# Kernel optimization log

Hardware: AMD Instinct MI355X
Metric: run time of the kernel (lower is better)

The kernel has to match this reference:

```python
import jax, jax.numpy as jnp
import numpy as np

H = 1024        # hidden_size
NH = 16         # num_heads
HD = H // NH    # head_dim
DFF = 4 * H
SCALE = HD ** -0.5
EPS = 1e-5


def _ln(x, g, b):
    m = jnp.mean(x, axis=-1, keepdims=True)
    v = jnp.var(x, axis=-1, keepdims=True)
    return (x - m) * jax.lax.rsqrt(v + EPS) * g + b


def _heads(t, B):
    # [B, S, H] -> [B, NH, S, HD]
    return t.reshape(B, -1, NH, HD).transpose(0, 2, 1, 3)


def _merge(t, B):
    # [B, NH, S, HD] -> [B, S, H]
    return t.transpose(0, 2, 1, 3).reshape(B, -1, H)


def _attn(q, k, v):
    s = jnp.einsum('bhqd,bhkd->bhqk', q, k) * SCALE
    p = jax.nn.softmax(s, axis=-1)
    p = jnp.nan_to_num(p, nan=0.0)
    return jnp.einsum('bhqk,bhkd->bhqd', p, v)


def setup_inputs() -> dict:
    key = jax.random.key(0)
    ks = jax.random.split(key, 16)
    std = (2.0 / (5 * H)) ** 0.5
    B, S, SI = 2, 2048, 256
    d = {
        'x': jax.random.normal(ks[0], (B, S, H), jnp.float32),
        'image_features': jax.random.normal(ks[1], (B, SI, H), jnp.float32),
    }
    names = ['sq', 'sk', 'sv', 'so', 'cq', 'ck', 'cv', 'co']
    for i, n in enumerate(names):
        d['W_' + n] = std * jax.random.normal(ks[2 + i], (H, H), jnp.float32)
        d['b_' + n] = jnp.zeros((H,), jnp.float32)
    d['W_ff1'] = std * jax.random.normal(ks[10], (H, DFF), jnp.float32)
    d['b_ff1'] = jnp.zeros((DFF,), jnp.float32)
    d['W_ff2'] = std * jax.random.normal(ks[11], (DFF, H), jnp.float32)
    d['b_ff2'] = jnp.zeros((H,), jnp.float32)
    for n in ['ln1', 'ln2', 'ln3']:
        d['g_' + n] = jnp.ones((H,), jnp.float32)
        d['b_' + n] = jnp.zeros((H,), jnp.float32)
    return d


def reference(x, image_features,
              W_sq, b_sq, W_sk, b_sk, W_sv, b_sv, W_so, b_so,
              W_cq, b_cq, W_ck, b_ck, W_cv, b_cv, W_co, b_co,
              W_ff1, b_ff1, W_ff2, b_ff2,
              g_ln1, b_ln1, g_ln2, b_ln2, g_ln3, b_ln3):
    B = x.shape[0]
    x = x * 0.1
    img = image_features * 0.1

    # --- self attention (pre-norm) ---
    nx = _ln(x, g_ln1, b_ln1)
    q = _heads(nx @ W_sq + b_sq, B)
    k = _heads(nx @ W_sk + b_sk, B)
    v = _heads(nx @ W_sv + b_sv, B)
    so = _merge(_attn(q, k, v), B) @ W_so + b_so
    x = x + so

    # --- cross attention (pre-norm) ---
    nx = _ln(x, g_ln2, b_ln2)
    q = _heads(nx @ W_cq + b_cq, B)
    k = _heads(img @ W_ck + b_ck, B)
    v = _heads(img @ W_cv + b_cv, B)
    co = _merge(_attn(q, k, v), B) @ W_co + b_co
    x = x + co

    # --- feed forward (pre-norm) ---
    nx = _ln(x, g_ln3, b_ln3)
    ff = jax.nn.gelu(nx @ W_ff1 + b_ff1, approximate=False) @ W_ff2 + b_ff2
    x = x + ff
    return x * 10.0
```

## Files before the change

### kernel.cpp

```cpp
#include <hip/hip_runtime.h>
#include <hip/hip_bf16.h>

typedef __bf16 bf16;
typedef __bf16 bf16x4 __attribute__((ext_vector_type(4)));
typedef __bf16 bf16x8 __attribute__((ext_vector_type(8)));
typedef float  f32x4  __attribute__((ext_vector_type(4)));
typedef float  f32x16 __attribute__((ext_vector_type(16)));
typedef int    int4v  __attribute__((ext_vector_type(4)));

#define H_DIM 1024
#define NHEAD 16
#define HD    64
#define QSCL 0.18033688011112042f

__device__ __forceinline__ void gload_lds16(const bf16* g, bf16* l) {
    __builtin_amdgcn_global_load_lds((const __attribute__((address_space(1))) void*)g,
                                     (__attribute__((address_space(3))) void*)l, 16, 0, 0);
}

__device__ __forceinline__ unsigned cvtpk_bf16(float lo, float hi) {
    unsigned r;
    asm volatile("v_cvt_pk_bf16_f32 %0, %1, %2" : "=v"(r) : "v"(lo), "v"(hi));
    return r;
}

__device__ __forceinline__ void wconv_body(const float* __restrict__ W,
                                           bf16* __restrict__ Wt, int K, int N,
                                           int bx, int by, int t) {
    __shared__ float tile[64][65];
    const int n0 = bx * 64, k0 = by * 64;
#pragma unroll
    for (int p = 0; p < 4; ++p) {
        int lin = p * 1024 + t * 4;
        int r = lin >> 6, c = lin & 63;
        f32x4 v = *(const f32x4*)(W + (size_t)(k0 + r) * N + n0 + c);
        tile[r][c]     = v[0];
        tile[r][c + 1] = v[1];
        tile[r][c + 2] = v[2];
        tile[r][c + 3] = v[3];
    }
    __syncthreads();
#pragma unroll
    for (int p = 0; p < 4; ++p) {
        int lin = p * 1024 + t * 4;
        int rn = lin >> 6, ck = lin & 63;
        bf16x4 o;
#pragma unroll
        for (int j = 0; j < 4; ++j) o[j] = (bf16)tile[ck + j][rn];
        *(bf16x4*)(Wt + (size_t)(n0 + rn) * K + k0 + ck) = o;
    }
}

__global__ __launch_bounds__(256) void wconv_kernel(const float* __restrict__ W,
                                                    bf16* __restrict__ Wt,
                                                    int K, int N) {
    wconv_body(W, Wt, K, N, blockIdx.x, blockIdx.y, threadIdx.x);
}

struct WPtrs { const float* w[8]; bf16* o[8]; };
__global__ __launch_bounds__(256) void wconv8_kernel(WPtrs p) {
    const int m = blockIdx.z;
    wconv_body(p.w[m], p.o[m], 1024, 1024, blockIdx.x, blockIdx.y, threadIdx.x);
}

__global__ __launch_bounds__(256) void ln_kernel(const float* __restrict__ in, float inScale,
                                                 const float* __restrict__ g,
                                                 const float* __restrict__ b,
                                                 bf16* __restrict__ out) {
    const int row = blockIdx.x, t = threadIdx.x;
    const float* p = in + (size_t)row * H_DIM;
    f32x4 v = *(const f32x4*)(p + t * 4);
    v *= inScale;
    float s1 = v[0] + v[1] + v[2] + v[3];
    float s2 = v[0] * v[0] + v[1] * v[1] + v[2] * v[2] + v[3] * v[3];
#pragma unroll
    for (int m = 1; m < 64; m <<= 1) {
        s1 += __shfl_xor(s1, m);
        s2 += __shfl_xor(s2, m);
    }
    __shared__ float red[8];
    const int wave = t >> 6;
    if ((t & 63) == 0) { red[wave * 2] = s1; red[wave * 2 + 1] = s2; }
    __syncthreads();
    s1 = red[0] + red[2] + red[4] + red[6];
    s2 = red[1] + red[3] + red[5] + red[7];
    float mean = s1 * (1.0f / H_DIM);
    float var  = s2 * (1.0f / H_DIM) - mean * mean;
    float inv  = rsqrtf(var + 1e-5f);
    f32x4 gg = *(const f32x4*)(g + t * 4);
    f32x4 bb = *(const f32x4*)(b + t * 4);
    bf16x4 o;
#pragma unroll
    for (int j = 0; j < 4; ++j) o[j] = (bf16)((v[j] - mean) * inv * gg[j] + bb[j]);
    *(bf16x4*)(out + (size_t)row * H_DIM + t * 4) = o;
}

__global__ __launch_bounds__(256) void cvt_scale_kernel(const float* __restrict__ in,
                                                        bf16* __restrict__ out,
                                                        float s, int n4) {
    int i = blockIdx.x * 256 + threadIdx.x;
    if (i < n4) {
        f32x4 v = *(const f32x4*)(in + (size_t)i * 4);
        bf16x4 o;
#pragma unroll
        for (int j = 0; j < 4; ++j) o[j] = (bf16)(v[j] * s);
        *(bf16x4*)(out + (size_t)i * 4) = o;
    }
}

template <int BM, int BN, int MODE, bool OUT_BF16, bool GELU_EPI, bool HAS_RES>
__global__ __launch_bounds__(256) void gemm_kernel(const bf16* __restrict__ A,
                                                   const bf16* __restrict__ Bt,
                                                   const float* __restrict__ bias1,
                                                   const float* __restrict__ bias2,
                                                   const float* __restrict__ bias3,
                                                   const float* __restrict__ res,
                                                   void* __restrict__ o1, void* __restrict__ o2,
                                                   void* __restrict__ o3,
                                                   int M, int N, int K,
                                                   float resScale, float outScale, int slog2) {
    constexpr int CHUNKS = (BM + BN) / 32;
    constexpr int WRR = BM / 2, WCC = BN / 2;
    constexpr int MI = WRR / 32, NJ = WCC / 32;
    __shared__ bf16 SM[2][(BM + BN) * 64];
    const int nwg = gridDim.x * gridDim.y;
    const int dlin = blockIdx.y * gridDim.x + blockIdx.x;
    const int id = (dlin & 7) * (nwg >> 3) + (dlin >> 3);
    const int bx = id % gridDim.x, by = id / gridDim.x;
    const int m0 = by * BM, n0 = bx * BN;
    const int tid = threadIdx.x;
    const int wave = tid >> 6, lane = tid & 63;
    const int l31 = lane & 31, l5 = lane >> 5;
    const int wr = wave >> 1, wc = wave & 1;
    const int sr = lane >> 3, sc8 = (lane & 7) * 8;
    const int sc8x = sc8 ^ (sr << 3);
    const int rxr = (l31 & 7) << 3;

    f32x16 acc[MI][NJ] = {};

    auto stage = [&](int buf, int k0) {
#pragma unroll
        for (int p = 0; p < CHUNKS; ++p) {
            const int rr = p * 32 + wave * 8 + sr;
            bf16* l = &SM[buf][0] + p * 2048 + wave * 512;
            const bf16* g = (p < BM / 32)
                ? (A  + (size_t)(m0 + rr) * K + k0 + sc8x)
                : (Bt + (size_t)(n0 + rr - BM) * K + k0 + sc8x);
            gload_lds16(g, l);
        }
    };

    stage(0, 0);
    __syncthreads();
    int buf = 0;
    for (int k0 = 0; k0 < K; k0 += 64) {
        if (k0 + 64 < K) stage(buf ^ 1, k0 + 64);
#pragma unroll
        for (int kk = 0; kk < 4; ++kk) {
            const int sa = (kk * 16 + l5 * 8) ^ rxr;
            bf16x8 af[MI], bfr[NJ];
#pragma unroll
            for (int i = 0; i < MI; ++i)
                af[i] = *(const bf16x8*)&SM[buf][(wr * WRR + i * 32 + l31) * 64 + sa];
#pragma unroll
            for (int j = 0; j < NJ; ++j)
                bfr[j] = *(const bf16x8*)&SM[buf][(BM + wc * WCC + j * 32 + l31) * 64 + sa];
#pragma unroll
            for (int i = 0; i < MI; ++i)
#pragma unroll
                for (int j = 0; j < NJ; ++j)
                    acc[i][j] = __builtin_amdgcn_mfma_f32_32x32x16_bf16(af[i], bfr[j], acc[i][j], 0, 0, 0);
        }
        __syncthreads();
        buf ^= 1;
    }

#pragma unroll
    for (int i = 0; i < MI; ++i) {
#pragma unroll
        for (int j = 0; j < NJ; ++j) {
            const int col = n0 + wc * WCC + j * 32 + l31;
            const int rbase = m0 + wr * WRR + i * 32 + l5 * 4;
            if (MODE == 0) {
                const float bv = bias1[col];
#pragma unroll
                for (int rq = 0; rq < 4; ++rq)
#pragma unroll
                    for (int rr = 0; rr < 4; ++rr) {
                        const int row = rbase + rq * 8 + rr;
                        const size_t idx = (size_t)row * N + col;
                        float v = acc[i][j][rq * 4 + rr] + bv;
                        if (HAS_RES) v += res[idx] * resScale;
                        if (GELU_EPI) v = 0.5f * v * (1.0f + erff(v * 0.70710678118654752f));
                        v *= outScale;
                        if (OUT_BF16) ((bf16*)o1)[idx] = (bf16)v;
                        else          ((float*)o1)[idx] = v;
                    }
            } else {
                const int sec = col >> 10, cl = col & 1023;
                const bool isV = (MODE == 1) ? (sec == 2) : (sec == 1);
                const float* bp = (MODE == 1) ? (sec == 0 ? bias1 : sec == 1 ? bias2 : bias3)
                                              : (sec == 0 ? bias1 : bias2);
                const float bv = bp[cl];
                if (!isV) {
                    bf16* dst = (MODE == 1) ? (sec == 0 ? (bf16*)o1 : (bf16*)o2) : (bf16*)o1;
                    const float sc = (MODE == 1 && sec == 0) ? outScale : 1.f;
#pragma unroll
                    for (int rq = 0; rq < 4; ++rq)
#pragma unroll
                        for (int rr = 0; rr < 4; ++rr) {
                            const int row = rbase + rq * 8 + rr;
                            dst[(size_t)row * H_DIM + cl] = (bf16)((acc[i][j][rq * 4 + rr] + bv) * sc);
                        }
                } else {
                    bf16* dst = (MODE == 1) ? (bf16*)o3 : (bf16*)o2;
                    const int S = 1 << slog2;
                    const int hI = cl >> 6, dI = cl & 63;
#pragma unroll
                    for (int rq = 0; rq < 4; ++rq) {
                        const int row0 = rbase + rq * 8;
                        const int bI = row0 >> slog2, s0 = row0 & (S - 1);
                        bf16x4 ov;
#pragma unroll
                        for (int rr = 0; rr < 4; ++rr) ov[rr] = (bf16)(acc[i][j][rq * 4 + rr] + bv);
                        *(bf16x4*)(dst + ((size_t)((bI * NHEAD + hI) * HD + dI)) * S + s0) = ov;
                    }
                }
            }
        }
    }
}

__global__ __launch_bounds__(256) void attn_kernel(const bf16* __restrict__ Qb,
                                                   const bf16* __restrict__ Kb,
                                                   const bf16* __restrict__ Vt_g,
                                                   bf16* __restrict__ Ob,
                                                   int SQ, int SK) {
    __shared__ bf16 SMEM[2][2][64 * 64];
    const int nwg = gridDim.x * gridDim.y;
    const int dlin = blockIdx.y * gridDim.x + blockIdx.x;
    const int id = (dlin & 7) * (nwg >> 3) + (dlin >> 3);
    const int NQ = gridDim.y;
    const int bh = id / NQ, qt = id - bh * NQ;
    const int b = bh >> 4, h = bh & 15;
    const int q0 = qt * 64;
    const int tid = threadIdx.x, wave = tid >> 6, lane = tid & 63;
    const int lr = lane & 15, lhi = lane >> 4;

    const bf16* qp = Qb + ((size_t)b * SQ + q0 + wave * 16 + lr) * H_DIM + h * HD;
    bf16x8 qf0 = *(const bf16x8*)(qp + lhi * 8);
    bf16x8 qf1 = *(const bf16x8*)(qp + 32 + lhi * 8);

    const int kx = (((lr & 3) | (((lr >> 2) & 1) << 2)) << 3);
    const int vx = (((lr & 3) | (((lr >> 3) & 1) << 2)) << 3);
    int krow[4];
#pragma unroll
    for (int nf = 0; nf < 4; ++nf)
        krow[nf] = (nf >> 1) * 32 + (lr >> 2) * 8 + (nf & 1) * 4 + (lr & 3);

    const int rS = tid >> 3, cS = (tid & 7) * 8;
    const int kxw = (((rS & 3) | (((rS >> 3) & 1) << 2)) << 3);
    const bf16* Kg = Kb + (size_t)b * SK * H_DIM + h * HD;
    const bf16* Vg = Vt_g + (size_t)bh * 64 * SK;

    bf16x8 onesv;
#pragma unroll
    for (int j = 0; j < 8; ++j) onesv[j] = (bf16)1.0f;

    f32x4 o[4] = {};
    f32x4 psum = {};
    bf16x8 gK[2], gV[2];

    auto LOADG = [&](int kb) {
#pragma unroll
        for (int p = 0; p < 2; ++p) {
            gK[p] = *(const bf16x8*)(Kg + (size_t)(kb + p * 32 + rS) * H_DIM + cS);
            gV[p] = *(const bf16x8*)(Vg + (size_t)(p * 32 + rS) * SK + kb + cS);
        }
    };
    auto STORES = [&](int buf) {
#pragma unroll
        for (int p = 0; p < 2; ++p) {
            *(bf16x8*)&SMEM[buf][0][(p * 32 + rS) * 64 + (cS ^ kxw)] = gK[p];
            *(bf16x8*)&SMEM[buf][1][(p * 32 + rS) * 64 + (cS ^ kxw)] = gV[p];
        }
    };
    auto COMPUTE = [&](int buf) {
        f32x4 s[4] = {};
#pragma unroll
        for (int nf = 0; nf < 4; ++nf) {
            const int base = krow[nf] * 64;
            bf16x8 kf0 = *(const bf16x8*)&SMEM[buf][0][base + ((lhi * 8) ^ kx)];
            bf16x8 kf1 = *(const bf16x8*)&SMEM[buf][0][base + ((32 + lhi * 8) ^ kx)];
            s[nf] = __builtin_amdgcn_mfma_f32_16x16x32_bf16(kf0, qf0, s[nf], 0, 0, 0);
            s[nf] = __builtin_amdgcn_mfma_f32_16x16x32_bf16(kf1, qf1, s[nf], 0, 0, 0);
        }
        unsigned pw[8];
#pragma unroll
        for (int nf = 0; nf < 4; ++nf) {
            float p0 = exp2f(s[nf][0]);
            float p1 = exp2f(s[nf][1]);
            float p2 = exp2f(s[nf][2]);
            float p3 = exp2f(s[nf][3]);
            pw[nf * 2]     = cvtpk_bf16(p0, p1);
            pw[nf * 2 + 1] = cvtpk_bf16(p2, p3);
        }
#pragma unroll
        for (int kk = 0; kk < 2; ++kk) {
            int4v w = { (int)pw[kk * 4], (int)pw[kk * 4 + 1],
                        (int)pw[kk * 4 + 2], (int)pw[kk * 4 + 3] };
            bf16x8 pb = __builtin_bit_cast(bf16x8, w);
            psum = __builtin_amdgcn_mfma_f32_16x16x32_bf16(onesv, pb, psum, 0, 0, 0);
#pragma unroll
            for (int df = 0; df < 4; ++df) {
                bf16x8 vf = *(const bf16x8*)&SMEM[buf][1][(df * 16 + lr) * 64 + ((kk * 32 + lhi * 8) ^ vx)];
                o[df] = __builtin_amdgcn_mfma_f32_16x16x32_bf16(vf, pb, o[df], 0, 0, 0);
            }
        }
    };

    const int nt = SK >> 6;
    LOADG(0);
    STORES(0);
    if (nt > 1) LOADG(64);
    __syncthreads();
    for (int t = 0; t < nt; ++t) {
        COMPUTE(t & 1);
        if (t + 1 < nt) {
            STORES((t + 1) & 1);
            if (t + 2 < nt) LOADG((t + 2) << 6);
        }
        __syncthreads();
    }

    bf16* T = &SMEM[0][0][0] + wave * (16 * 72);
    const float inv = 1.0f / psum[0];
#pragma unroll
    for (int df = 0; df < 4; ++df)
#pragma unroll
        for (int r = 0; r < 4; ++r)
            T[lr * 72 + df * 16 + lhi * 4 + r] = (bf16)(o[df][r] * inv);
#pragma unroll
    for (int pp = 0; pp < 2; ++pp) {
        const int r16 = pp * 8 + (lane >> 3), ch = (lane & 7) * 8;
        bf16x8 v = *(const bf16x8*)&T[r16 * 72 + ch];
        *(bf16x8*)(Ob + ((size_t)b * SQ + q0 + wave * 16 + r16) * H_DIM + h * HD + ch) = v;
    }
}

extern "C" void kernel_launch(void* const* d_in, const int* in_sizes, int n_in,
                              void* d_out, int out_size, void* d_ws, size_t ws_size,
                              hipStream_t stream) {
    const float* x    = (const float*)d_in[0];
    const float* img  = (const float*)d_in[1];
    const float* W_sq = (const float*)d_in[2];   const float* b_sq = (const float*)d_in[3];
    const float* W_sk = (const float*)d_in[4];   const float* b_sk = (const float*)d_in[5];
    const float* W_sv = (const float*)d_in[6];   const float* b_sv = (const float*)d_in[7];
    const float* W_so = (const float*)d_in[8];   const float* b_so = (const float*)d_in[9];
    const float* W_cq = (const float*)d_in[10];  const float* b_cq = (const float*)d_in[11];
    const float* W_ck = (const float*)d_in[12];  const float* b_ck = (const float*)d_in[13];
    const float* W_cv = (const float*)d_in[14];  const float* b_cv = (const float*)d_in[15];
    const float* W_co = (const float*)d_in[16];  const float* b_co = (const float*)d_in[17];
    const float* W_f1 = (const float*)d_in[18];  const float* b_f1 = (const float*)d_in[19];
    const float* W_f2 = (const float*)d_in[20];  const float* b_f2 = (const float*)d_in[21];
    const float* g1 = (const float*)d_in[22];    const float* bb1 = (const float*)d_in[23];
    const float* g2 = (const float*)d_in[24];    const float* bb2 = (const float*)d_in[25];
    const float* g3 = (const float*)d_in[26];    const float* bb3 = (const float*)d_in[27];

    char* ws = (char*)d_ws;
    const size_t MB = 1ull << 20;
    bf16* WT   = (bf16*)ws;
    bf16* w_sq = WT + 0 * (1u << 20);
    bf16* w_sk = WT + 1 * (1u << 20);
    bf16* w_sv = WT + 2 * (1u << 20);
    bf16* w_so = WT + 3 * (1u << 20);
    bf16* w_cq = WT + 4 * (1u << 20);
    bf16* w_ck = WT + 5 * (1u << 20);
    bf16* w_cv = WT + 6 * (1u << 20);
    bf16* w_co = WT + 7 * (1u << 20);
    bf16* w_f1 = WT + 8 * (1u << 20);
    bf16* w_f2 = WT + 12 * (1u << 20);
    float* XR  = (float*)(ws + 32 * MB);
    bf16* NX   = (bf16*)(ws + 48 * MB);
    bf16* Qb   = (bf16*)(ws + 56 * MB);
    bf16* Kb   = (bf16*)(ws + 64 * MB);
    bf16* Vt   = (bf16*)(ws + 72 * MB);
    bf16* FF   = (bf16*)(ws + 56 * MB);
    bf16* IMGB = (bf16*)(ws + 88 * MB);

    const dim3 blk(256);

    WPtrs wp;
    wp.w[0] = W_sq; wp.o[0] = w_sq;  wp.w[1] = W_sk; wp.o[1] = w_sk;
    wp.w[2] = W_sv; wp.o[2] = w_sv;  wp.w[3] = W_so; wp.o[3] = w_so;
    wp.w[4] = W_cq; wp.o[4] = w_cq;  wp.w[5] = W_ck; wp.o[5] = w_ck;
    wp.w[6] = W_cv; wp.o[6] = w_cv;  wp.w[7] = W_co; wp.o[7] = w_co;
    wconv8_kernel<<<dim3(16, 16, 8), blk, 0, stream>>>(wp);
    wconv_kernel<<<dim3(64, 16), blk, 0, stream>>>(W_f1, w_f1, 1024, 4096);
    wconv_kernel<<<dim3(16, 64), blk, 0, stream>>>(W_f2, w_f2, 4096, 1024);

    ln_kernel<<<4096, blk, 0, stream>>>(x, 0.1f, g1, bb1, NX);
    gemm_kernel<128, 128, 1, true, false, false><<<dim3(24, 32), blk, 0, stream>>>(
        NX, w_sq, b_sq, b_sk, b_sv, nullptr, Qb, Kb, Vt, 4096, 3072, 1024, 0.f, QSCL, 11);
    attn_kernel<<<dim3(32, 32), blk, 0, stream>>>(Qb, Kb, Vt, NX, 2048, 2048);
    gemm_kernel<64, 128, 0, false, false, true><<<dim3(8, 64), blk, 0, stream>>>(
        NX, w_so, b_so, nullptr, nullptr, x, XR, nullptr, nullptr, 4096, 1024, 1024, 0.1f, 1.f, 0);

    ln_kernel<<<4096, blk, 0, stream>>>(XR, 1.f, g2, bb2, NX);
    gemm_kernel<64, 128, 0, true, false, false><<<dim3(8, 64), blk, 0, stream>>>(
        NX, w_cq, b_cq, nullptr, nullptr, nullptr, Qb, nullptr, nullptr, 4096, 1024, 1024, 0.f, QSCL, 0);
    cvt_scale_kernel<<<dim3(512), blk, 0, stream>>>(img, IMGB, 0.1f, 131072);
    gemm_kernel<64, 128, 2, true, false, false><<<dim3(16, 8), blk, 0, stream>>>(
        IMGB, w_ck, b_ck, b_cv, nullptr, nullptr, Kb, Vt, nullptr, 512, 2048, 1024, 0.f, 1.f, 8);
    attn_kernel<<<dim3(32, 32), blk, 0, stream>>>(Qb, Kb, Vt, NX, 2048, 256);
    gemm_kernel<64, 128, 0, false, false, true><<<dim3(8, 64), blk, 0, stream>>>(
        NX, w_co, b_co, nullptr, nullptr, XR, XR, nullptr, nullptr, 4096, 1024, 1024, 1.f, 1.f, 0);

    ln_kernel<<<4096, blk, 0, stream>>>(XR, 1.f, g3, bb3, NX);
    gemm_kernel<128, 128, 0, true, true, false><<<dim3(32, 32), blk, 0, stream>>>(
        NX, w_f1, b_f1, nullptr, nullptr, nullptr, FF, nullptr, nullptr, 4096, 4096, 1024, 0.f, 1.f, 0);
    gemm_kernel<64, 128, 0, false, false, true><<<dim3(8, 64), blk, 0, stream>>>(
        FF, w_f2, b_f2, nullptr, nullptr, XR, d_out, nullptr, nullptr, 4096, 1024, 4096, 1.f, 10.f, 0);
}
```

Measured before the change: 305.8 us.

## Process 128 query rows per attention block to reuse K/V tiles

Each attention workgroup now covers 128 query rows, 32 per wave as two 16-row fragments, instead of 64. Every K/V tile staged in LDS feeds twice as many MFMAs, halving K/V global traffic and LDS staging per query. The grid is halved to 512 blocks, which lowers parallelism on a 256-CU device, and the larger accumulator state raises register pressure and may cut occupancy.

Measured after the change: 304.0 us. About the same (-0.6%).

```diff
diff --git a/kernel.cpp b/kernel.cpp
--- a/kernel.cpp
+++ b/kernel.cpp
@@ -243,13 +243,17 @@
     const int NQ = gridDim.y;
     const int bh = id / NQ, qt = id - bh * NQ;
     const int b = bh >> 4, h = bh & 15;
-    const int q0 = qt * 64;
+    const int q0 = qt * 128;
     const int tid = threadIdx.x, wave = tid >> 6, lane = tid & 63;
     const int lr = lane & 15, lhi = lane >> 4;
 
-    const bf16* qp = Qb + ((size_t)b * SQ + q0 + wave * 16 + lr) * H_DIM + h * HD;
-    bf16x8 qf0 = *(const bf16x8*)(qp + lhi * 8);
-    bf16x8 qf1 = *(const bf16x8*)(qp + 32 + lhi * 8);
+    bf16x8 qf[2][2];
+#pragma unroll
+    for (int qi = 0; qi < 2; ++qi) {
+        const bf16* qp = Qb + ((size_t)b * SQ + q0 + wave * 32 + qi * 16 + lr) * H_DIM + h * HD;
+        qf[qi][0] = *(const bf16x8*)(qp + lhi * 8);
+        qf[qi][1] = *(const bf16x8*)(qp + 32 + lhi * 8);
+    }
 
     const int kx = (((lr & 3) | (((lr >> 2) & 1) << 2)) << 3);
     const int vx = (((lr & 3) | (((lr >> 3) & 1) << 2)) << 3);
@@ -267,8 +271,8 @@
 #pragma unroll
     for (int j = 0; j < 8; ++j) onesv[j] = (bf16)1.0f;
 
-    f32x4 o[4] = {};
-    f32x4 psum = {};
+    f32x4 o[2][4] = {};
+    f32x4 psum[2] = {};
     bf16x8 gK[2], gV[2];
 
     auto LOADG = [&](int kb) {
@@ -286,35 +290,45 @@
         }
     };
     auto COMPUTE = [&](int buf) {
-        f32x4 s[4] = {};
+        f32x4 s[2][4] = {};
 #pragma unroll
         for (int nf = 0; nf < 4; ++nf) {
             const int base = krow[nf] * 64;
             bf16x8 kf0 = *(const bf16x8*)&SMEM[buf][0][base + ((lhi * 8) ^ kx)];
             bf16x8 kf1 = *(const bf16x8*)&SMEM[buf][0][base + ((32 + lhi * 8) ^ kx)];
-            s[nf] = __builtin_amdgcn_mfma_f32_16x16x32_bf16(kf0, qf0, s[nf], 0, 0, 0);
-            s[nf] = __builtin_amdgcn_mfma_f32_16x16x32_bf16(kf1, qf1, s[nf], 0, 0, 0);
-        }
-        unsigned pw[8];
-#pragma unroll
-        for (int nf = 0; nf < 4; ++nf) {
-            float p0 = exp2f(s[nf][0]);
-            float p1 = exp2f(s[nf][1]);
-            float p2 = exp2f(s[nf][2]);
-            float p3 = exp2f(s[nf][3]);
-            pw[nf * 2]     = cvtpk_bf16(p0, p1);
-            pw[nf * 2 + 1] = cvtpk_bf16(p2, p3);
-        }
+#pragma unroll
+            for (int qi = 0; qi < 2; ++qi) {
+                s[qi][nf] = __builtin_amdgcn_mfma_f32_16x16x32_bf16(kf0, qf[qi][0], s[qi][nf], 0, 0, 0);
+                s[qi][nf] = __builtin_amdgcn_mfma_f32_16x16x32_bf16(kf1, qf[qi][1], s[qi][nf], 0, 0, 0);
+            }
+        }
+        unsigned pw[2][8];
+#pragma unroll
+        for (int qi = 0; qi < 2; ++qi)
+#pragma unroll
+            for (int nf = 0; nf < 4; ++nf) {
+                float p0 = exp2f(s[qi][nf][0]);
+                float p1 = exp2f(s[qi][nf][1]);
+                float p2 = exp2f(s[qi][nf][2]);
+                float p3 = exp2f(s[qi][nf][3]);
+                pw[qi][nf * 2]     = cvtpk_bf16(p0, p1);
+                pw[qi][nf * 2 + 1] = cvtpk_bf16(p2, p3);
+            }
 #pragma unroll
         for (int kk = 0; kk < 2; ++kk) {
-            int4v w = { (int)pw[kk * 4], (int)pw[kk * 4 + 1],
-                        (int)pw[kk * 4 + 2], (int)pw[kk * 4 + 3] };
-            bf16x8 pb = __builtin_bit_cast(bf16x8, w);
-            psum = __builtin_amdgcn_mfma_f32_16x16x32_bf16(onesv, pb, psum, 0, 0, 0);
+            bf16x8 pb[2];
+#pragma unroll
+            for (int qi = 0; qi < 2; ++qi) {
+                int4v w = { (int)pw[qi][kk * 4], (int)pw[qi][kk * 4 + 1],
+                            (int)pw[qi][kk * 4 + 2], (int)pw[qi][kk * 4 + 3] };
+                pb[qi] = __builtin_bit_cast(bf16x8, w);
+                psum[qi] = __builtin_amdgcn_mfma_f32_16x16x32_bf16(onesv, pb[qi], psum[qi], 0, 0, 0);
+            }
 #pragma unroll
             for (int df = 0; df < 4; ++df) {
                 bf16x8 vf = *(const bf16x8*)&SMEM[buf][1][(df * 16 + lr) * 64 + ((kk * 32 + lhi * 8) ^ vx)];
-                o[df] = __builtin_amdgcn_mfma_f32_16x16x32_bf16(vf, pb, o[df], 0, 0, 0);
+                o[0][df] = __builtin_amdgcn_mfma_f32_16x16x32_bf16(vf, pb[0], o[0][df], 0, 0, 0);
+                o[1][df] = __builtin_amdgcn_mfma_f32_16x16x32_bf16(vf, pb[1], o[1][df], 0, 0, 0);
             }
         }
     };
@@ -333,18 +347,21 @@
         __syncthreads();
     }
 
-    bf16* T = &SMEM[0][0][0] + wave * (16 * 72);
-    const float inv = 1.0f / psum[0];
-#pragma unroll
-    for (int df = 0; df < 4; ++df)
-#pragma unroll
-        for (int r = 0; r < 4; ++r)
-            T[lr * 72 + df * 16 + lhi * 4 + r] = (bf16)(o[df][r] * inv);
-#pragma unroll
-    for (int pp = 0; pp < 2; ++pp) {
-        const int r16 = pp * 8 + (lane >> 3), ch = (lane & 7) * 8;
-        bf16x8 v = *(const bf16x8*)&T[r16 * 72 + ch];
-        *(bf16x8*)(Ob + ((size_t)b * SQ + q0 + wave * 16 + r16) * H_DIM + h * HD + ch) = v;
+    bf16* T = &SMEM[0][0][0] + wave * (32 * 72);
+#pragma unroll
+    for (int qi = 0; qi < 2; ++qi) {
+        const float inv = 1.0f / psum[qi][0];
+#pragma unroll
+        for (int df = 0; df < 4; ++df)
+#pragma unroll
+            for (int r = 0; r < 4; ++r)
+                T[(qi * 16 + lr) * 72 + df * 16 + lhi * 4 + r] = (bf16)(o[qi][df][r] * inv);
+    }
+#pragma unroll
+    for (int pp = 0; pp < 4; ++pp) {
+        const int r32 = pp * 8 + (lane >> 3), ch = (lane & 7) * 8;
+        bf16x8 v = *(const bf16x8*)&T[r32 * 72 + ch];
+        *(bf16x8*)(Ob + ((size_t)b * SQ + q0 + wave * 32 + r32) * H_DIM + h * HD + ch) = v;
     }
 }
 
@@ -402,7 +419,7 @@
     ln_kernel<<<4096, blk, 0, stream>>>(x, 0.1f, g1, bb1, NX);
     gemm_kernel<128, 128, 1, true, false, false><<<dim3(24, 32), blk, 0, stream>>>(
         NX, w_sq, b_sq, b_sk, b_sv, nullptr, Qb, Kb, Vt, 4096, 3072, 1024, 0.f, QSCL, 11);
-    attn_kernel<<<dim3(32, 32), blk, 0, stream>>>(Qb, Kb, Vt, NX, 2048, 2048);
+    attn_kernel<<<dim3(32, 16), blk, 0, stream>>>(Qb, Kb, Vt, NX, 2048, 2048);
     gemm_kernel<64, 128, 0, false, false, true><<<dim3(8, 64), blk, 0, stream>>>(
         NX, w_so, b_so, nullptr, nullptr, x, XR, nullptr, nullptr, 4096, 1024, 1024, 0.1f, 1.f, 0);
 
@@ -412,7 +429,7 @@
     cvt_scale_kernel<<<dim3(512), blk, 0, stream>>>(img, IMGB, 0.1f, 131072);
     gemm_kernel<64, 128, 2, true, false, false><<<dim3(16, 8), blk, 0, stream>>>(
         IMGB, w_ck, b_ck, b_cv, nullptr, nullptr, Kb, Vt, nullptr, 512, 2048, 1024, 0.f, 1.f, 8);
-    attn_kernel<<<dim3(32, 32), blk, 0, stream>>>(Qb, Kb, Vt, NX, 2048, 256);
+    attn_kernel<<<dim3(32, 16), blk, 0, stream>>>(Qb, Kb, Vt, NX, 2048, 256);
     gemm_kernel<64, 128, 0, false, false, true><<<dim3(8, 64), blk, 0, stream>>>(
         NX, w_co, b_co, nullptr, nullptr, XR, XR, nullptr, nullptr, 4096, 1024, 1024, 1.f, 1.f, 0);
 
```
